# Kernel optimization log

Hardware: AMD Instinct MI355X
Metric: run time of the kernel (lower is better)

The kernel has to match this reference:

```python
import jax, jax.numpy as jnp
import numpy as np
import math

K_S = 2  # graph power order
K_T = 2  # temporal localization copies
BN_EPS = 1e-5


def setup_inputs() -> dict:
    key = jax.random.key(0)
    ks = jax.random.split(key, 12)
    B, L, N, H, ND = 8, 12, 1024, 32, 16
    AF = H + ND  # all_feat_dim
    return {
        "history_data": jax.random.normal(ks[0], (B, L, N, 1), jnp.float32),
        "node_embedding_d": jax.random.normal(ks[1], (N, ND), jnp.float32),
        "node_embedding_u": jax.random.normal(ks[2], (N, ND), jnp.float32),
        "adj0": jax.random.uniform(ks[3], (N, N), jnp.float32),
        "adj1": jax.random.uniform(ks[4], (N, N), jnp.float32),
        "W1": jax.random.normal(ks[5], (L, 2 * H), jnp.float32) * 0.1,
        "b1": jnp.zeros((2 * H,), jnp.float32),
        "gamma": jnp.ones((2 * H,), jnp.float32),
        "beta": jnp.zeros((2 * H,), jnp.float32),
        "W2": jax.random.normal(ks[6], (2 * H, H), jnp.float32) * 0.1,
        "b2": jnp.zeros((H,), jnp.float32),
        "WQ": jax.random.normal(ks[7], (AF, H), jnp.float32) * 0.1,
        "WK": jax.random.normal(ks[8], (AF, H), jnp.float32) * 0.1,
    }


def _forward(history_data, node_embedding_d, node_embedding_u, adj0, adj1,
             W1, b1, gamma, beta, W2, b2, WQ, WK):
    B, L, N, _ = history_data.shape
    H = W2.shape[1]

    # --- DistanceFunction ---
    X = jnp.transpose(history_data[..., 0], (0, 2, 1)).reshape(B * N, L)  # [B*N, L]
    h = jax.nn.relu(X @ W1 + b1)                                          # [B*N, 2H]
    mu = jnp.mean(h, axis=0)
    var = jnp.var(h, axis=0)  # biased, matches torch BatchNorm1d train norm
    h = (h - mu) * jax.lax.rsqrt(var + BN_EPS) * gamma + beta
    dy_feat = (h @ W2 + b2).reshape(B, N, H)                              # [B, N, H]

    scale = 1.0 / math.sqrt(H)
    adjs = []
    for emb in (node_embedding_d, node_embedding_u):
        feat = jnp.concatenate(
            [dy_feat, jnp.broadcast_to(emb[None], (B,) + emb.shape)], axis=-1)
        Q = feat @ WQ  # [B, N, H]
        K = feat @ WK
        logits = jnp.einsum("bnh,bmh->bnm", Q, K) * scale
        adjs.append(jax.nn.softmax(logits, axis=-1))

    # --- Mask ---
    adjs = [(adj0 + 1e-7)[None] * adjs[0], (adj1 + 1e-7)[None] * adjs[1]]

    # --- Normalizer: diag_embed+bmm is just a row-wise broadcast scale ---
    def norm(g):
        inv = 1.0 / jnp.sum(g, axis=2)
        inv = jnp.where(jnp.isfinite(inv), inv, 0.0)
        return inv[:, :, None] * g
    adjs = [norm(g) for g in adjs]

    # --- MultiOrder (k=1..K_S), zero diagonal ---
    offdiag = 1.0 - jnp.eye(N, dtype=adjs[0].dtype)
    graphs = []
    for g in adjs:
        k_order = g
        graphs.append(k_order * offdiag)
        for _ in range(2, K_S + 1):
            k_order = jnp.einsum("bnm,bmk->bnk", k_order, g)
            graphs.append(k_order * offdiag)

    # --- st_localization: [B,N,N] -> [B,N,K_T*N] (row repeated K_T times) ---
    local = [jnp.broadcast_to(g[:, :, None, :], (B, N, K_T, N)).reshape(B, N, K_T * N)
             for g in graphs]
    return jnp.stack(local, axis=0)  # [2*K_S, B, N, K_T*N]


def reference(history_data, node_embedding_d, node_embedding_u, adj0, adj1,
              W1, b1, gamma, beta, W2, b2, WQ, WK):
    return _forward(history_data, node_embedding_d, node_embedding_u, adj0, adj1,
                    W1, b1, gamma, beta, W2, b2, WQ, WK)
```

## Files before the change

### kernel.cpp

```cpp
#include <hip/hip_runtime.h>

typedef unsigned short u16;
typedef unsigned int   u32;

typedef __bf16 bf16x8 __attribute__((ext_vector_type(8)));
typedef float  f32x4  __attribute__((ext_vector_type(4)));

__device__ __forceinline__ float bf2f(u16 u) {
  u32 x = ((u32)u) << 16; float f; __builtin_memcpy(&f, &x, 4); return f;
}
__device__ __forceinline__ u16 f2bf(float f) {
  u32 x; __builtin_memcpy(&x, &f, 4);
  x += 0x7fffu + ((x >> 16) & 1u);
  return (u16)(x >> 16);
}
__device__ __forceinline__ void gl2lds16(const void* g, void* l) {
  __builtin_amdgcn_global_load_lds((const __attribute__((address_space(1))) void*)g,
                                   (__attribute__((address_space(3))) void*)l, 16, 0, 0);
}

__global__ __launch_bounds__(256) void k_h(const float* __restrict__ hd, const float* __restrict__ W1,
                                           const float* __restrict__ b1, float* __restrict__ h)
{
  __shared__ float w1s[12 * 64];
  __shared__ float b1s[64];
  int t = threadIdx.x;
  for (int idx = t; idx < 768; idx += 256) w1s[idx] = W1[idx];
  if (t < 64) b1s[t] = b1[t];
  __syncthreads();
  int i = blockIdx.x * 256 + t;
  int b = i >> 10, n = i & 1023;
  float x[12];
#pragma unroll
  for (int l = 0; l < 12; ++l) x[l] = hd[(b * 12 + l) * 1024 + n];
  float acc[64];
#pragma unroll
  for (int j = 0; j < 64; ++j) acc[j] = b1s[j];
#pragma unroll
  for (int l = 0; l < 12; ++l) {
    float xl = x[l];
#pragma unroll
    for (int j = 0; j < 64; ++j) acc[j] += xl * w1s[l * 64 + j];
  }
  float4* hv = (float4*)(h + (size_t)i * 64);
#pragma unroll
  for (int j4 = 0; j4 < 16; ++j4) {
    float4 v;
    v.x = fmaxf(acc[j4 * 4 + 0], 0.f);
    v.y = fmaxf(acc[j4 * 4 + 1], 0.f);
    v.z = fmaxf(acc[j4 * 4 + 2], 0.f);
    v.w = fmaxf(acc[j4 * 4 + 3], 0.f);
    hv[j4] = v;
  }
}

__global__ __launch_bounds__(256) void k_stats(const float* __restrict__ h, float* __restrict__ stats)
{
  int t = threadIdx.x;
  size_t base = (size_t)blockIdx.x * 8192;
  float s = 0.f, sq = 0.f;
  for (int it = 0; it < 32; ++it) {
    float v = h[base + it * 256 + t];
    s += v; sq += v * v;
  }
  __shared__ float ls[256], lq[256];
  ls[t] = s; lq[t] = sq;
  __syncthreads();
  if (t < 64) {
    float S = ls[t] + ls[t + 64] + ls[t + 128] + ls[t + 192];
    float Q = lq[t] + lq[t + 64] + lq[t + 128] + lq[t + 192];
    atomicAdd(&stats[t], S);
    atomicAdd(&stats[64 + t], Q);
  }
}

__global__ void k_finalize(const float* __restrict__ stats, const float* __restrict__ gamma,
                           const float* __restrict__ beta, float* __restrict__ ss)
{
  int t = threadIdx.x;
  float mu = stats[t] * (1.f / 8192.f);
  float var = stats[64 + t] * (1.f / 8192.f) - mu * mu;
  float inv = rsqrtf(var + 1e-5f);
  float sc = gamma[t] * inv;
  ss[t] = sc;
  ss[64 + t] = beta[t] - mu * sc;
}

__global__ __launch_bounds__(256) void k_emb(const float* __restrict__ embd, const float* __restrict__ embu,
                                             const float* __restrict__ WQ, const float* __restrict__ WK,
                                             float* __restrict__ embpart)
{
  int g = blockIdx.x * 256 + threadIdx.x;
  int o = g & 31, n = (g >> 5) & 1023, qk = (g >> 15) & 1, e = g >> 16;
  const float* emb = e ? embu : embd;
  const float* W = qk ? WK : WQ;
  float acc = 0.f;
#pragma unroll
  for (int d = 0; d < 16; ++d) acc += emb[n * 16 + d] * W[(32 + d) * 32 + o];
  embpart[g] = acc;
}

__global__ __launch_bounds__(256) void k_dyqk(const float* __restrict__ h, const float* __restrict__ ss,
                                              const float* __restrict__ W2, const float* __restrict__ b2,
                                              const float* __restrict__ WQ, const float* __restrict__ WK,
                                              const float* __restrict__ embpart,
                                              float* __restrict__ QTf, u16* __restrict__ KTb)
{
  __shared__ float w2s[64 * 32], wqs[32 * 32], wks[32 * 32], b2s[32], scs[64], shs[64];
  int t = threadIdx.x;
  for (int idx = t; idx < 2048; idx += 256) w2s[idx] = W2[idx];
  for (int idx = t; idx < 1024; idx += 256) { wqs[idx] = WQ[idx]; wks[idx] = WK[idx]; }
  if (t < 32) b2s[t] = b2[t];
  if (t < 64) { scs[t] = ss[t]; shs[t] = ss[64 + t]; }
  __syncthreads();
  int i = blockIdx.x * 256 + t;
  int b = i >> 10, n = i & 1023;
  float dy[32];
#pragma unroll
  for (int o = 0; o < 32; ++o) dy[o] = b2s[o];
  for (int j = 0; j < 64; ++j) {
    float hj = h[(size_t)i * 64 + j] * scs[j] + shs[j];
#pragma unroll
    for (int o = 0; o < 32; ++o) dy[o] += hj * w2s[j * 32 + o];
  }
  float tq[32], tk[32];
#pragma unroll
  for (int o = 0; o < 32; ++o) { tq[o] = 0.f; tk[o] = 0.f; }
  for (int j = 0; j < 32; ++j) {
    float d = dy[j];
#pragma unroll
    for (int o = 0; o < 32; ++o) { tq[o] += d * wqs[j * 32 + o]; tk[o] += d * wks[j * 32 + o]; }
  }
#pragma unroll
  for (int e = 0; e < 2; ++e) {
    const float* epQ = embpart + ((size_t)(e * 2 + 0) * 1024 + n) * 32;
    const float* epK = embpart + ((size_t)(e * 2 + 1) * 1024 + n) * 32;
    size_t qb = ((size_t)(e * 8 + b) * 32) * 1024 + n;
#pragma unroll
    for (int o = 0; o < 32; ++o) {
      QTf[qb + (size_t)o * 1024] = tq[o] + epQ[o];
      KTb[qb + (size_t)o * 1024] = f2bf(tk[o] + epK[o]);
    }
  }
}

__global__ __launch_bounds__(256) void k_attn(const float* __restrict__ QTf, const u16* __restrict__ KTb,
                                              const float* __restrict__ adj0, const float* __restrict__ adj1,
                                              u16* __restrict__ G, float* __restrict__ out)
{
  int blk = (blockIdx.x & 7) * 64 + (blockIdx.x >> 3);
  int rg = blk & 31, b = (blk >> 5) & 7, e = blk >> 8;
  int t = threadIdx.x;
  int eb = e * 8 + b;
  int wv = t >> 6, lane = t & 63;
  const float* adj = e ? adj1 : adj0;
  const u16* Kp = KTb + ((size_t)eb << 15);
  const float* Qp = QTf + ((size_t)eb << 15);
  u16* Gp = G + ((size_t)eb << 20);
  float* o1 = out + (((size_t)(2 * e) * 8 + b) << 21);
  const float sc = 0.17677669529663687f;
#pragma unroll
  for (int grp = 0; grp < 2; ++grp) {
    int r0 = rg * 32 + wv * 8 + grp * 4;
    float accA[4][8], accB[4][8];
#pragma unroll
    for (int r = 0; r < 4; ++r)
#pragma unroll
      for (int k = 0; k < 8; ++k) { accA[r][k] = 0.f; accB[r][k] = 0.f; }
    for (int hh = 0; hh < 32; ++hh) {
      float4 qv = *(const float4*)(Qp + hh * 1024 + r0);
      uint4 ka = *(const uint4*)(Kp + hh * 1024 + lane * 8);
      uint4 kb = *(const uint4*)(Kp + hh * 1024 + 512 + lane * 8);
      float kf[8] = {bf2f((u16)ka.x), bf2f((u16)(ka.x >> 16)), bf2f((u16)ka.y), bf2f((u16)(ka.y >> 16)),
                     bf2f((u16)ka.z), bf2f((u16)(ka.z >> 16)), bf2f((u16)ka.w), bf2f((u16)(ka.w >> 16))};
      float kg[8] = {bf2f((u16)kb.x), bf2f((u16)(kb.x >> 16)), bf2f((u16)kb.y), bf2f((u16)(kb.y >> 16)),
                     bf2f((u16)kb.z), bf2f((u16)(kb.z >> 16)), bf2f((u16)kb.w), bf2f((u16)(kb.w >> 16))};
#pragma unroll
      for (int k = 0; k < 8; ++k) {
        accA[0][k] += qv.x * kf[k]; accA[1][k] += qv.y * kf[k];
        accA[2][k] += qv.z * kf[k]; accA[3][k] += qv.w * kf[k];
        accB[0][k] += qv.x * kg[k]; accB[1][k] += qv.y * kg[k];
        accB[2][k] += qv.z * kg[k]; accB[3][k] += qv.w * kg[k];
      }
    }
#pragma unroll
    for (int r = 0; r < 4; ++r) {
      int gr = r0 + r;
      const float* arow = adj + ((size_t)gr << 10);
      int mA = lane * 8, mB = 512 + lane * 8;
      float4 a0 = *(const float4*)(arow + mA);
      float4 a1 = *(const float4*)(arow + mA + 4);
      float4 c0 = *(const float4*)(arow + mB);
      float4 c1 = *(const float4*)(arow + mB + 4);
      float af[8] = {a0.x, a0.y, a0.z, a0.w, a1.x, a1.y, a1.z, a1.w};
      float bfv[8] = {c0.x, c0.y, c0.z, c0.w, c1.x, c1.y, c1.z, c1.w};
      float ta[8], tb[8];
      float p = 0.f;
#pragma unroll
      for (int k = 0; k < 8; ++k) { ta[k] = (af[k] + 1e-7f) * __expf(accA[r][k] * sc); p += ta[k]; }
#pragma unroll
      for (int k = 0; k < 8; ++k) { tb[k] = (bfv[k] + 1e-7f) * __expf(accB[r][k] * sc); p += tb[k]; }
#pragma unroll
      for (int off = 32; off > 0; off >>= 1) p += __shfl_xor(p, off);
      float inv = 1.f / p;
      if (!__builtin_isfinite(inv)) inv = 0.f;
      float ga[8], gb[8];
#pragma unroll
      for (int k = 0; k < 8; ++k) { ga[k] = ta[k] * inv; gb[k] = tb[k] * inv; }
      uint4 pa, pb;
      pa.x = f2bf(ga[0]) | ((u32)f2bf(ga[1]) << 16);  pa.y = f2bf(ga[2]) | ((u32)f2bf(ga[3]) << 16);
      pa.z = f2bf(ga[4]) | ((u32)f2bf(ga[5]) << 16);  pa.w = f2bf(ga[6]) | ((u32)f2bf(ga[7]) << 16);
      pb.x = f2bf(gb[0]) | ((u32)f2bf(gb[1]) << 16);  pb.y = f2bf(gb[2]) | ((u32)f2bf(gb[3]) << 16);
      pb.z = f2bf(gb[4]) | ((u32)f2bf(gb[5]) << 16);  pb.w = f2bf(gb[6]) | ((u32)f2bf(gb[7]) << 16);
      *(uint4*)(Gp + ((size_t)gr << 10) + mA) = pa;
      *(uint4*)(Gp + ((size_t)gr << 10) + mB) = pb;
#pragma unroll
      for (int k = 0; k < 8; ++k) {
        if (mA + k == gr) ga[k] = 0.f;
        if (mB + k == gr) gb[k] = 0.f;
      }
      size_t ob = (size_t)gr << 11;
      float4 fa0 = {ga[0], ga[1], ga[2], ga[3]}, fa1 = {ga[4], ga[5], ga[6], ga[7]};
      float4 fb0 = {gb[0], gb[1], gb[2], gb[3]}, fb1 = {gb[4], gb[5], gb[6], gb[7]};
      *(float4*)(o1 + ob + mA) = fa0;         *(float4*)(o1 + ob + mA + 4) = fa1;
      *(float4*)(o1 + ob + mB) = fb0;         *(float4*)(o1 + ob + mB + 4) = fb1;
      *(float4*)(o1 + ob + 1024 + mA) = fa0;  *(float4*)(o1 + ob + 1024 + mA + 4) = fa1;
      *(float4*)(o1 + ob + 1024 + mB) = fb0;  *(float4*)(o1 + ob + 1024 + mB + 4) = fb1;
    }
  }
}

__global__ __launch_bounds__(256) void k_tr(const u16* __restrict__ G, u16* __restrict__ Gt)
{
  __shared__ u16 tile[64 * 66];
  int blk = blockIdx.x;
  int mat = blk >> 8, tl = blk & 255, ti = tl >> 4, tj = tl & 15;
  size_t mo = (size_t)mat << 20;
  int t = threadIdx.x;
#pragma unroll
  for (int half = 0; half < 2; ++half) {
    int idx = t + half * 256;
    int row = idx >> 3, q = idx & 7;
    uint4 v = *(const uint4*)(G + mo + (size_t)(ti * 64 + row) * 1024 + tj * 64 + q * 8);
    u16* d = &tile[row * 66 + q * 8];
    d[0] = (u16)v.x; d[1] = (u16)(v.x >> 16);
    d[2] = (u16)v.y; d[3] = (u16)(v.y >> 16);
    d[4] = (u16)v.z; d[5] = (u16)(v.z >> 16);
    d[6] = (u16)v.w; d[7] = (u16)(v.w >> 16);
  }
  __syncthreads();
#pragma unroll
  for (int half = 0; half < 2; ++half) {
    int idx = t + half * 256;
    int row = idx >> 3, q = idx & 7;
    u16 s0 = tile[(q * 8 + 0) * 66 + row], s1 = tile[(q * 8 + 1) * 66 + row];
    u16 s2 = tile[(q * 8 + 2) * 66 + row], s3 = tile[(q * 8 + 3) * 66 + row];
    u16 s4 = tile[(q * 8 + 4) * 66 + row], s5 = tile[(q * 8 + 5) * 66 + row];
    u16 s6 = tile[(q * 8 + 6) * 66 + row], s7 = tile[(q * 8 + 7) * 66 + row];
    uint4 v;
    v.x = s0 | ((u32)s1 << 16); v.y = s2 | ((u32)s3 << 16);
    v.z = s4 | ((u32)s5 << 16); v.w = s6 | ((u32)s7 << 16);
    *(uint4*)(Gt + mo + (size_t)(tj * 64 + row) * 1024 + ti * 64 + q * 8) = v;
  }
}

__global__ __launch_bounds__(256) void k_gemm(const u16* __restrict__ G, const u16* __restrict__ Gt,
                                              float* __restrict__ out)
{
  __shared__ __align__(16) u16 As[128 * 32];
  __shared__ __align__(16) u16 Bs[128 * 32];
  __shared__ __align__(16) float tile[32 * 132];
  int bid = (blockIdx.x & 7) * 128 + (blockIdx.x >> 3);
  int mat = bid >> 6, tl = bid & 63, ti = tl >> 3, tj = tl & 7;
  size_t mo = (size_t)mat << 20;
  const u16* A = G + mo;
  const u16* Bm = Gt + mo;
  int t = threadIdx.x;
  int w = t >> 6, lane = t & 63;
  int quad = lane >> 4, l16 = lane & 15;
  int wr = (w & 1) * 64, wc = (w >> 1) * 64;
  f32x4 acc[4][4];
#pragma unroll
  for (int i = 0; i < 4; ++i)
#pragma unroll
    for (int j = 0; j < 4; ++j) acc[i][j] = f32x4{0.f, 0.f, 0.f, 0.f};
  for (int k0 = 0; k0 < 1024; k0 += 32) {
#pragma unroll
    for (int it = 0; it < 2; ++it) {
      int sbase = (it * 4 + w) * 64;
      int s = sbase + lane;
      int r = s >> 2, c = s & 3;
      gl2lds16(A + (size_t)(ti * 128 + r) * 1024 + k0 + c * 8, (u16*)As + (size_t)sbase * 8);
      gl2lds16(Bm + (size_t)(tj * 128 + r) * 1024 + k0 + c * 8, (u16*)Bs + (size_t)sbase * 8);
    }
    __syncthreads();
    bf16x8 af[4], bfr[4];
#pragma unroll
    for (int mt = 0; mt < 4; ++mt)
      af[mt] = *(const bf16x8*)&As[(wr + mt * 16 + l16) * 32 + quad * 8];
#pragma unroll
    for (int nt = 0; nt < 4; ++nt)
      bfr[nt] = *(const bf16x8*)&Bs[(wc + nt * 16 + l16) * 32 + quad * 8];
#pragma unroll
    for (int mt = 0; mt < 4; ++mt)
#pragma unroll
      for (int nt = 0; nt < 4; ++nt)
        acc[mt][nt] = __builtin_amdgcn_mfma_f32_16x16x32_bf16(af[mt], bfr[nt], acc[mt][nt], 0, 0, 0);
    __syncthreads();
  }
  int e = mat >> 3, bb = mat & 7;
  float* o2 = out + (((size_t)(2 * e + 1) * 8 + bb) << 21);
  int lrbase = (w & 1) * 16 + quad * 4;
#pragma unroll
  for (int mt = 0; mt < 4; ++mt) {
    __syncthreads();
#pragma unroll
    for (int nt = 0; nt < 4; ++nt)
#pragma unroll
      for (int r = 0; r < 4; ++r)
        tile[(lrbase + r) * 132 + wc + nt * 16 + l16] = acc[mt][nt][r];
    __syncthreads();
#pragma unroll
    for (int it = 0; it < 4; ++it) {
      int idx = it * 256 + t;
      int lr = idx >> 5, c4 = idx & 31;
      float4 v = *(const float4*)&tile[lr * 132 + c4 * 4];
      int gr = ti * 128 + (lr >> 4) * 64 + mt * 16 + (lr & 15);
      int gc0 = tj * 128 + c4 * 4;
      if (gr == gc0 + 0) v.x = 0.f;
      if (gr == gc0 + 1) v.y = 0.f;
      if (gr == gc0 + 2) v.z = 0.f;
      if (gr == gc0 + 3) v.w = 0.f;
      size_t rb = (size_t)gr << 11;
      *(float4*)(o2 + rb + gc0) = v;
      *(float4*)(o2 + rb + 1024 + gc0) = v;
    }
  }
}

extern "C" void kernel_launch(void* const* d_in, const int* in_sizes, int n_in,
                              void* d_out, int out_size, void* d_ws, size_t ws_size,
                              hipStream_t stream) {
  const float* hd    = (const float*)d_in[0];
  const float* embd  = (const float*)d_in[1];
  const float* embu  = (const float*)d_in[2];
  const float* adj0  = (const float*)d_in[3];
  const float* adj1  = (const float*)d_in[4];
  const float* W1    = (const float*)d_in[5];
  const float* b1    = (const float*)d_in[6];
  const float* gamma = (const float*)d_in[7];
  const float* beta  = (const float*)d_in[8];
  const float* W2    = (const float*)d_in[9];
  const float* b2    = (const float*)d_in[10];
  const float* WQ    = (const float*)d_in[11];
  const float* WK    = (const float*)d_in[12];
  char* ws = (char*)d_ws;
  float* stats   = (float*)(ws + 0);
  float* ss      = (float*)(ws + 1024);
  float* embpart = (float*)(ws + 4096);
  float* h       = (float*)(ws + 528384);
  float* QTf     = (float*)(ws + 2625536);
  u16* KTb       = (u16*)(ws + 4722688);
  u16* G         = (u16*)(ws + 5771264);
  u16* Gt        = (u16*)(ws + 39325696);
  float* out     = (float*)d_out;

  hipMemsetAsync(stats, 0, 512, stream);
  k_h<<<32, 256, 0, stream>>>(hd, W1, b1, h);
  k_stats<<<64, 256, 0, stream>>>(h, stats);
  k_finalize<<<1, 64, 0, stream>>>(stats, gamma, beta, ss);
  k_emb<<<512, 256, 0, stream>>>(embd, embu, WQ, WK, embpart);
  k_dyqk<<<32, 256, 0, stream>>>(h, ss, W2, b2, WQ, WK, embpart, QTf, KTb);
  k_attn<<<512, 256, 0, stream>>>(QTf, KTb, adj0, adj1, G, out);
  k_tr<<<4096, 256, 0, stream>>>(G, Gt);
  k_gemm<<<1024, 256, 0, stream>>>(G, Gt, out);
}
```

Before: 425.8 us.

## Fuse transpose of normalized graph into attention kernel via LDS tile

The attention kernel now stages each block's 32 rows of bf16 normalized adjacency into shared memory and writes the transposed columns directly to Gt. This removes the separate transpose kernel, along with its full re-read of G from global memory and one launch. In exchange it adds about 33 KB of LDS per block, extra registers to hold the second-half values, and two block barriers in k_attn. The transposed stores are 64-byte row segments, which may be less coalesced than before.

After: 442.0 us. +3.8%, slower.

```diff
diff --git a/kernel.cpp b/kernel.cpp
--- a/kernel.cpp
+++ b/kernel.cpp
@@ -146,8 +146,10 @@
 
 __global__ __launch_bounds__(256) void k_attn(const float* __restrict__ QTf, const u16* __restrict__ KTb,
                                               const float* __restrict__ adj0, const float* __restrict__ adj1,
-                                              u16* __restrict__ G, float* __restrict__ out)
-{
+                                              u16* __restrict__ G, u16* __restrict__ Gt,
+                                              float* __restrict__ out)
+{
+  __shared__ u16 tile[32 * 516];
   int blk = (blockIdx.x & 7) * 64 + (blockIdx.x >> 3);
   int rg = blk & 31, b = (blk >> 5) & 7, e = blk >> 8;
   int t = threadIdx.x;
@@ -157,8 +159,10 @@
   const u16* Kp = KTb + ((size_t)eb << 15);
   const float* Qp = QTf + ((size_t)eb << 15);
   u16* Gp = G + ((size_t)eb << 20);
+  u16* Gtp = Gt + ((size_t)eb << 20);
   float* o1 = out + (((size_t)(2 * e) * 8 + b) << 21);
   const float sc = 0.17677669529663687f;
+  uint4 pbs[2][4];
 #pragma unroll
   for (int grp = 0; grp < 2; ++grp) {
     int r0 = rg * 32 + wv * 8 + grp * 4;
@@ -214,6 +218,8 @@
       pb.z = f2bf(gb[4]) | ((u32)f2bf(gb[5]) << 16);  pb.w = f2bf(gb[6]) | ((u32)f2bf(gb[7]) << 16);
       *(uint4*)(Gp + ((size_t)gr << 10) + mA) = pa;
       *(uint4*)(Gp + ((size_t)gr << 10) + mB) = pb;
+      *(uint4*)&tile[(wv * 8 + grp * 4 + r) * 516 + mA] = pa;
+      pbs[grp][r] = pb;
 #pragma unroll
       for (int k = 0; k < 8; ++k) {
         if (mA + k == gr) ga[k] = 0.f;
@@ -228,39 +234,35 @@
       *(float4*)(o1 + ob + 1024 + mB) = fb0;  *(float4*)(o1 + ob + 1024 + mB + 4) = fb1;
     }
   }
-}
-
-__global__ __launch_bounds__(256) void k_tr(const u16* __restrict__ G, u16* __restrict__ Gt)
-{
-  __shared__ u16 tile[64 * 66];
-  int blk = blockIdx.x;
-  int mat = blk >> 8, tl = blk & 255, ti = tl >> 4, tj = tl & 15;
-  size_t mo = (size_t)mat << 20;
-  int t = threadIdx.x;
-#pragma unroll
-  for (int half = 0; half < 2; ++half) {
-    int idx = t + half * 256;
-    int row = idx >> 3, q = idx & 7;
-    uint4 v = *(const uint4*)(G + mo + (size_t)(ti * 64 + row) * 1024 + tj * 64 + q * 8);
-    u16* d = &tile[row * 66 + q * 8];
-    d[0] = (u16)v.x; d[1] = (u16)(v.x >> 16);
-    d[2] = (u16)v.y; d[3] = (u16)(v.y >> 16);
-    d[4] = (u16)v.z; d[5] = (u16)(v.z >> 16);
-    d[6] = (u16)v.w; d[7] = (u16)(v.w >> 16);
-  }
-  __syncthreads();
-#pragma unroll
-  for (int half = 0; half < 2; ++half) {
-    int idx = t + half * 256;
-    int row = idx >> 3, q = idx & 7;
-    u16 s0 = tile[(q * 8 + 0) * 66 + row], s1 = tile[(q * 8 + 1) * 66 + row];
-    u16 s2 = tile[(q * 8 + 2) * 66 + row], s3 = tile[(q * 8 + 3) * 66 + row];
-    u16 s4 = tile[(q * 8 + 4) * 66 + row], s5 = tile[(q * 8 + 5) * 66 + row];
-    u16 s6 = tile[(q * 8 + 6) * 66 + row], s7 = tile[(q * 8 + 7) * 66 + row];
-    uint4 v;
-    v.x = s0 | ((u32)s1 << 16); v.y = s2 | ((u32)s3 << 16);
-    v.z = s4 | ((u32)s5 << 16); v.w = s6 | ((u32)s7 << 16);
-    *(uint4*)(Gt + mo + (size_t)(tj * 64 + row) * 1024 + ti * 64 + q * 8) = v;
+  for (int ph = 0; ph < 2; ++ph) {
+    if (ph) {
+      __syncthreads();
+#pragma unroll
+      for (int g2 = 0; g2 < 2; ++g2)
+#pragma unroll
+        for (int r = 0; r < 4; ++r)
+          *(uint4*)&tile[(wv * 8 + g2 * 4 + r) * 516 + lane * 8] = pbs[g2][r];
+    }
+    __syncthreads();
+    int c0 = t * 2;
+    u32 v[32];
+#pragma unroll
+    for (int r = 0; r < 32; ++r) v[r] = *(const u32*)&tile[r * 516 + c0];
+    u32 w0[16], w1[16];
+#pragma unroll
+    for (int i = 0; i < 16; ++i) {
+      w0[i] = (v[2 * i] & 0xffffu) | (v[2 * i + 1] << 16);
+      w1[i] = (v[2 * i] >> 16) | (v[2 * i + 1] & 0xffff0000u);
+    }
+    u16* d0 = Gtp + (size_t)(ph * 512 + c0) * 1024 + rg * 32;
+    u16* d1 = d0 + 1024;
+#pragma unroll
+    for (int i = 0; i < 4; ++i) {
+      uint4 q0 = {w0[4 * i], w0[4 * i + 1], w0[4 * i + 2], w0[4 * i + 3]};
+      uint4 q1 = {w1[4 * i], w1[4 * i + 1], w1[4 * i + 2], w1[4 * i + 3]};
+      *(uint4*)(d0 + i * 8) = q0;
+      *(uint4*)(d1 + i * 8) = q1;
+    }
   }
 }
 
@@ -371,7 +373,6 @@
   k_finalize<<<1, 64, 0, stream>>>(stats, gamma, beta, ss);
   k_emb<<<512, 256, 0, stream>>>(embd, embu, WQ, WK, embpart);
   k_dyqk<<<32, 256, 0, stream>>>(h, ss, W2, b2, WQ, WK, embpart, QTf, KTb);
-  k_attn<<<512, 256, 0, stream>>>(QTf, KTb, adj0, adj1, G, out);
-  k_tr<<<4096, 256, 0, stream>>>(G, Gt);
+  k_attn<<<512, 256, 0, stream>>>(QTf, KTb, adj0, adj1, G, Gt, out);
   k_gemm<<<1024, 256, 0, stream>>>(G, Gt, out);
 }
```
